# Kernel optimization log

Hardware: AMD Instinct MI355X
Metric: run time of the kernel (lower is better)

The kernel has to match this reference:

```python
import jax, jax.numpy as jnp
import numpy as np

BETA = 0.999      # EMA momentum from __init__ default
MIN_PTS = 256     # per-class minimum point count from forward()
EPS = 1e-12       # torch F.normalize eps


def _l2norm(v):
    n = jnp.sqrt(jnp.sum(v * v, axis=1, keepdims=True))
    return v / jnp.maximum(n, EPS)


def setup_inputs() -> dict:
    key = jax.random.key(0)
    ks = jax.random.split(key, 14)
    B, N, CIN = 4, 40000, 4
    ENC_H, ENC_D, PROJ_H, PRIOR_D, NC = 256, 512, 256, 128, 13
    s = 0.02
    pos = jax.random.normal(ks[0], (B, N, 3), jnp.float32)
    x = jax.random.normal(ks[1], (B, CIN, N), jnp.float32)
    y = jax.random.randint(ks[2], (B, N), 0, NC)
    # pointwise encoder stand-in (real encoder is an opaque external PointNeXt)
    W_enc1 = jax.random.normal(ks[3], (CIN + 3, ENC_H), jnp.float32) * s
    b_enc1 = jnp.zeros((ENC_H,), jnp.float32)
    W_enc2 = jax.random.normal(ks[4], (ENC_H, ENC_D), jnp.float32) * s
    b_enc2 = jnp.zeros((ENC_D,), jnp.float32)
    # projection head: Linear(512->256) ReLU Linear(256->128) ReLU
    W1 = jax.random.normal(ks[5], (ENC_D, PROJ_H), jnp.float32) * s
    b1 = jnp.zeros((PROJ_H,), jnp.float32)
    W2 = jax.random.normal(ks[6], (PROJ_H, PRIOR_D), jnp.float32) * s
    b2 = jnp.zeros((PRIOR_D,), jnp.float32)
    prior_ema = _l2norm(jax.random.uniform(ks[7], (NC, PRIOR_D), jnp.float32))
    return {"pos": pos, "x": x, "y": y,
            "W_enc1": W_enc1, "b_enc1": b_enc1, "W_enc2": W_enc2, "b_enc2": b_enc2,
            "W1": W1, "b1": b1, "W2": W2, "b2": b2, "prior_ema": prior_ema}


def reference(pos, x, y, W_enc1, b_enc1, W_enc2, b_enc2, W1, b1, W2, b2, prior_ema):
    NC = prior_ema.shape[0]
    p0 = pos.reshape(-1, pos.shape[-1])                       # [P, 3]
    f0 = jnp.transpose(x, (0, 2, 1)).reshape(-1, x.shape[1])  # [P, C]
    labels = y.reshape(-1)                                    # [P]
    # per-class counts and the >=256 validity gate (replaces the Python class loop)
    counts = jax.ops.segment_sum(jnp.ones(labels.shape, jnp.float32), labels, num_segments=NC)
    valid = counts >= MIN_PTS                                 # [NC]
    # encoder stand-in: pointwise MLP on (features, coords)
    h = jax.nn.relu(jnp.concatenate([f0, p0], axis=1) @ W_enc1 + b_enc1)
    enc = jax.nn.relu(h @ W_enc2 + b_enc2)                    # [P, 512]
    # projection head + L2 normalize
    g = jax.nn.relu(enc @ W1 + b1)
    feat = jax.nn.relu(g @ W2 + b2)                           # [P, 128]
    feat = _l2norm(feat)
    # current_prior: features + float label column (-1 marks dropped classes)
    lbl_eff = jnp.where(valid[labels], labels, -1)
    current_prior = jnp.concatenate([feat, lbl_eff[:, None].astype(feat.dtype)], axis=1)
    # _ema: detached per-class segment mean, keep old prior for empty/invalid classes
    fsg = jax.lax.stop_gradient(feat)
    sums = jax.ops.segment_sum(fsg, labels, num_segments=NC)  # [NC, 128]
    means = sums / jnp.maximum(counts, 1.0)[:, None]
    cur = jnp.where(valid[:, None], means, prior_ema)
    new_prior = _l2norm(BETA * prior_ema + (1.0 - BETA) * cur)
    return current_prior, new_prior
```

## Files before the change

### kernel.cpp

```cpp
#include <hip/hip_runtime.h>
#include <hip/hip_bf16.h>

#define P_TOTAL 160000
#define NPB     40000
#define NCLS    13
#define TP      64
#define NBLK    (P_TOTAL / TP)

typedef __attribute__((ext_vector_type(8))) short bf16x8;
typedef __attribute__((ext_vector_type(4))) float f32x4;

__device__ __forceinline__ ushort f2bf(float f) {
  union { float f; unsigned u; } v; v.f = f;
  return (ushort)((v.u + 0x8000) >> 16);
}

__device__ __forceinline__ void transpose_tile(const float* __restrict__ src,
                                               ushort* __restrict__ dst,
                                               int K, int N, int tile, ushort (*t)[33]) {
  int ntx = N >> 5;
  int n0 = (tile % ntx) << 5, k0 = (tile / ntx) << 5;
  int c = threadIdx.x & 31, r = threadIdx.x >> 5;
  #pragma unroll
  for (int rr = 0; rr < 32; rr += 8)
    t[r + rr][c] = f2bf(src[(k0 + r + rr) * N + n0 + c]);
  __syncthreads();
  #pragma unroll
  for (int rr = 0; rr < 32; rr += 8)
    dst[(n0 + r + rr) * K + k0 + c] = t[c][r + rr];
}

__global__ void prep_all_kernel(const float* __restrict__ We1, const float* __restrict__ We2,
                                const float* __restrict__ W1,  const float* __restrict__ W2,
                                const int* __restrict__ y,
                                ushort* __restrict__ WT1, ushort* __restrict__ WT2,
                                ushort* __restrict__ WT3, ushort* __restrict__ WT4,
                                int* __restrict__ counts) {
  __shared__ ushort t[32][33];
  __shared__ int h[NCLS];
  int b = blockIdx.x, tid = threadIdx.x;
  if (b < 128)       transpose_tile(We2, WT2, 256, 512, b, t);
  else if (b < 256)  transpose_tile(W1,  WT3, 512, 256, b - 128, t);
  else if (b < 288)  transpose_tile(W2,  WT4, 256, 128, b - 256, t);
  else if (b == 288) {
    for (int i = tid; i < 8192; i += 256) {
      int n = i >> 5, k = i & 31;
      WT1[i] = (k < 7) ? f2bf(We1[k * 256 + n]) : (ushort)0;
    }
  } else {
    if (tid < NCLS) h[tid] = 0;
    __syncthreads();
    for (int i = (b - 289) * 256 + tid; i < P_TOTAL; i += 127 * 256)
      atomicAdd(&h[y[i]], 1);
    __syncthreads();
    if (tid < NCLS) atomicAdd(&counts[tid], h[tid]);
  }
}

__global__ __launch_bounds__(512, 4) void main_kernel(
    const float* __restrict__ pos, const float* __restrict__ x, const int* __restrict__ y,
    const float* __restrict__ be1, const float* __restrict__ be2,
    const float* __restrict__ b1,  const float* __restrict__ b2,
    const ushort* __restrict__ WT1, const ushort* __restrict__ WT2,
    const ushort* __restrict__ WT3, const ushort* __restrict__ WT4,
    const int* __restrict__ counts, float* __restrict__ gsums, int* __restrict__ done,
    const float* __restrict__ prior, float* __restrict__ out) {
  __shared__ ushort actbuf[TP * 264];
  __shared__ ushort chunk2[2][TP * 136];
  __shared__ float  part[8 * TP];
  __shared__ float  inv_norm[TP];
  __shared__ float  lbl_eff[TP];
  __shared__ int    lbl[TP];
  __shared__ float  invn[NCLS];
  __shared__ int    is_last;

  const int tid  = threadIdx.x;
  const int wave = tid >> 6, lane = tid & 63;
  const int quad = lane >> 4, mrow = lane & 15;
  const long p0 = (long)blockIdx.x * TP;
  const int bb = (int)(p0 / NPB);
  const int n0 = (int)(p0 % NPB);
  const f32x4 zero = {0.f, 0.f, 0.f, 0.f};

  for (int i = tid; i < TP * 40; i += 512) {
    int r = i / 40, k = i - r * 40;
    float v = 0.f;
    if (k < 4)      v = x[(bb * 4 + k) * NPB + n0 + r];
    else if (k < 7) v = pos[(p0 + r) * 3 + (k - 4)];
    chunk2[0][r * 40 + k] = f2bf(v);
  }
  if (tid < TP) lbl[tid] = y[p0 + tid];
  __syncthreads();

  {
    f32x4 acc1[4][2];
    #pragma unroll
    for (int mt = 0; mt < 4; mt++) { acc1[mt][0] = zero; acc1[mt][1] = zero; }
    const int kl = quad << 3;
    bf16x8 af[4], bw[2];
    #pragma unroll
    for (int mt = 0; mt < 4; mt++)
      af[mt] = *(const bf16x8*)(&chunk2[0][0] + (mt * 16 + mrow) * 40 + kl);
    #pragma unroll
    for (int nt = 0; nt < 2; nt++)
      bw[nt] = *(const bf16x8*)(WT1 + (wave * 32 + nt * 16 + mrow) * 32 + kl);
    #pragma unroll
    for (int nt = 0; nt < 2; nt++)
      #pragma unroll
      for (int mt = 0; mt < 4; mt++)
        acc1[mt][nt] = __builtin_amdgcn_mfma_f32_16x16x32_bf16(af[mt], bw[nt], acc1[mt][nt], 0, 0, 0);
    #pragma unroll
    for (int nt = 0; nt < 2; nt++) {
      int n = wave * 32 + nt * 16 + mrow;
      float bv = be1[n];
      #pragma unroll
      for (int mt = 0; mt < 4; mt++)
        #pragma unroll
        for (int r = 0; r < 4; r++)
          actbuf[(mt * 16 + quad * 4 + r) * 264 + n] = f2bf(fmaxf(acc1[mt][nt][r] + bv, 0.f));
    }
  }
  __syncthreads();

  f32x4 acc3[4][2];
  #pragma unroll
  for (int mt = 0; mt < 4; mt++) { acc3[mt][0] = zero; acc3[mt][1] = zero; }

  for (int c = 0; c < 4; c++) {
    ushort* cb = &chunk2[c & 1][0];
    f32x4 acc2[4];
    #pragma unroll
    for (int mt = 0; mt < 4; mt++) acc2[mt] = zero;
    #pragma unroll
    for (int ks = 0; ks < 8; ks++) {
      const int kl = ks * 32 + (quad << 3);
      bf16x8 af[4];
      #pragma unroll
      for (int mt = 0; mt < 4; mt++)
        af[mt] = *(const bf16x8*)(actbuf + (mt * 16 + mrow) * 264 + kl);
      bf16x8 bw = *(const bf16x8*)(WT2 + (long)(c * 128 + wave * 16 + mrow) * 256 + kl);
      #pragma unroll
      for (int mt = 0; mt < 4; mt++)
        acc2[mt] = __builtin_amdgcn_mfma_f32_16x16x32_bf16(af[mt], bw, acc2[mt], 0, 0, 0);
    }
    {
      int lc = wave * 16 + mrow;
      float bv = be2[c * 128 + lc];
      #pragma unroll
      for (int mt = 0; mt < 4; mt++)
        #pragma unroll
        for (int r = 0; r < 4; r++)
          cb[(mt * 16 + quad * 4 + r) * 136 + lc] = f2bf(fmaxf(acc2[mt][r] + bv, 0.f));
    }
    __syncthreads();
    #pragma unroll
    for (int ks = 0; ks < 4; ks++) {
      const int kl = ks * 32 + (quad << 3);
      bf16x8 af[4], bw[2];
      #pragma unroll
      for (int mt = 0; mt < 4; mt++)
        af[mt] = *(const bf16x8*)(cb + (mt * 16 + mrow) * 136 + kl);
      #pragma unroll
      for (int nt = 0; nt < 2; nt++)
        bw[nt] = *(const bf16x8*)(WT3 + (long)(wave * 32 + nt * 16 + mrow) * 512 + c * 128 + kl);
      #pragma unroll
      for (int nt = 0; nt < 2; nt++)
        #pragma unroll
        for (int mt = 0; mt < 4; mt++)
          acc3[mt][nt] = __builtin_amdgcn_mfma_f32_16x16x32_bf16(af[mt], bw[nt], acc3[mt][nt], 0, 0, 0);
    }
  }

  #pragma unroll
  for (int nt = 0; nt < 2; nt++) {
    int n = wave * 32 + nt * 16 + mrow;
    float bv = b1[n];
    #pragma unroll
    for (int mt = 0; mt < 4; mt++)
      #pragma unroll
      for (int r = 0; r < 4; r++)
        actbuf[(mt * 16 + quad * 4 + r) * 264 + n] = f2bf(fmaxf(acc3[mt][nt][r] + bv, 0.f));
  }
  __syncthreads();

  f32x4 acc4[4];
  #pragma unroll
  for (int mt = 0; mt < 4; mt++) acc4[mt] = zero;
  #pragma unroll
  for (int ks = 0; ks < 8; ks++) {
    const int kl = ks * 32 + (quad << 3);
    bf16x8 af[4];
    #pragma unroll
    for (int mt = 0; mt < 4; mt++)
      af[mt] = *(const bf16x8*)(actbuf + (mt * 16 + mrow) * 264 + kl);
    bf16x8 bw = *(const bf16x8*)(WT4 + (long)(wave * 16 + mrow) * 256 + kl);
    #pragma unroll
    for (int mt = 0; mt < 4; mt++)
      acc4[mt] = __builtin_amdgcn_mfma_f32_16x16x32_bf16(af[mt], bw, acc4[mt], 0, 0, 0);
  }
  const int col = wave * 16 + mrow;
  float val[4][4];
  {
    float bv = b2[col];
    #pragma unroll
    for (int mt = 0; mt < 4; mt++)
      #pragma unroll
      for (int r = 0; r < 4; r++)
        val[mt][r] = fmaxf(acc4[mt][r] + bv, 0.f);
  }

  #pragma unroll
  for (int mt = 0; mt < 4; mt++)
    #pragma unroll
    for (int r = 0; r < 4; r++) {
      float s = val[mt][r] * val[mt][r];
      s += __shfl_xor(s, 1);  s += __shfl_xor(s, 2);
      s += __shfl_xor(s, 4);  s += __shfl_xor(s, 8);
      if (mrow == 0) part[wave * TP + mt * 16 + quad * 4 + r] = s;
    }
  __syncthreads();
  if (tid < TP) {
    float ss = 0.f;
    #pragma unroll
    for (int w = 0; w < 8; w++) ss += part[w * TP + tid];
    inv_norm[tid] = 1.f / fmaxf(sqrtf(ss), 1e-12f);
    int l = lbl[tid];
    lbl_eff[tid] = (counts[l] >= 256) ? (float)l : -1.f;
  }
  __syncthreads();

  float a[NCLS];
  #pragma unroll
  for (int cc = 0; cc < NCLS; cc++) a[cc] = 0.f;
  #pragma unroll
  for (int mt = 0; mt < 4; mt++)
    #pragma unroll
    for (int r = 0; r < 4; r++) {
      int R = mt * 16 + quad * 4 + r;
      float vn = val[mt][r] * inv_norm[R];
      out[(p0 + R) * 129 + col] = vn;
      int cls = lbl[R];
      #pragma unroll
      for (int cc = 0; cc < NCLS; cc++) a[cc] += (cls == cc) ? vn : 0.f;
    }
  if (tid < TP) out[(p0 + tid) * 129 + 128] = lbl_eff[tid];
  #pragma unroll
  for (int cc = 0; cc < NCLS; cc++) {
    a[cc] += __shfl_xor(a[cc], 16);
    a[cc] += __shfl_xor(a[cc], 32);
  }
  if (quad == 0)
    #pragma unroll
    for (int cc = 0; cc < NCLS; cc++) atomicAdd(&gsums[cc * 128 + col], a[cc]);

  __syncthreads();
  if (tid == 0) {
    int old = atomicAdd(done, 1);
    is_last = (old == NBLK - 1);
  }
  __syncthreads();
  if (!is_last) return;

  float* vbuf = (float*)actbuf;
  for (int i = tid; i < NCLS * 128; i += 512) {
    float g = atomicAdd(&gsums[i], 0.f);
    int cls = i >> 7;
    int cnt = counts[cls];
    float mean = g / fmaxf((float)cnt, 1.f);
    float pr = prior[i];
    float cur = (cnt >= 256) ? mean : pr;
    vbuf[i] = 0.999f * pr + 0.001f * cur;
  }
  __syncthreads();
  if (tid < NCLS) {
    float s = 0.f;
    for (int c = 0; c < 128; c++) { float t = vbuf[tid * 128 + c]; s += t * t; }
    invn[tid] = 1.f / fmaxf(sqrtf(s), 1e-12f);
  }
  __syncthreads();
  for (int i = tid; i < NCLS * 128; i += 512)
    out[(long)P_TOTAL * 129 + i] = vbuf[i] * invn[i >> 7];
}

extern "C" void kernel_launch(void* const* d_in, const int* in_sizes, int n_in,
                              void* d_out, int out_size, void* d_ws, size_t ws_size,
                              hipStream_t stream) {
  const float* pos   = (const float*)d_in[0];
  const float* x     = (const float*)d_in[1];
  const int*   y     = (const int*)  d_in[2];
  const float* We1   = (const float*)d_in[3];
  const float* be1   = (const float*)d_in[4];
  const float* We2   = (const float*)d_in[5];
  const float* be2   = (const float*)d_in[6];
  const float* W1    = (const float*)d_in[7];
  const float* b1    = (const float*)d_in[8];
  const float* W2    = (const float*)d_in[9];
  const float* b2    = (const float*)d_in[10];
  const float* prior = (const float*)d_in[11];
  float* out = (float*)d_out;

  char* ws = (char*)d_ws;
  int*    counts = (int*)   (ws + 0);
  float*  gsums  = (float*) (ws + 256);
  int*    done   = (int*)   (ws + 7168);
  ushort* WT1    = (ushort*)(ws + 8192);
  ushort* WT2    = (ushort*)(ws + 24576);
  ushort* WT3    = (ushort*)(ws + 286720);
  ushort* WT4    = (ushort*)(ws + 548864);

  hipMemsetAsync(ws, 0, 8192, stream);
  prep_all_kernel<<<416, 256, 0, stream>>>(We1, We2, W1, W2, y, WT1, WT2, WT3, WT4, counts);
  main_kernel    <<<NBLK, 512, 0, stream>>>(pos, x, y, be1, be2, b1, b2,
                                            WT1, WT2, WT3, WT4, counts, gsums, done, prior, out);
}
```

Baseline: 347.1 us.

## Switch middle GEMMs to 32x32x16 MFMA with wider chunks and LDS class sums

The encoder-layer-2 and projection-layer-1 GEMMs now use 32x32x16 bf16 MFMA instead of 16x16x32 and work in two 256-wide chunks rather than four 128-wide ones. Each weight fragment feeds two MFMAs, and a single full-width LDS buffer replaces the double-buffered chunk buffers, at the cost of an extra barrier between chunks. The per-class segment sums no longer use per-thread 13-register accumulators with shuffles. Instead they go through LDS atomics into a block-local table, which is flushed to global with sparse atomics. This aims to cut register pressure and global atomic traffic, but risks LDS atomic contention.

Measured after the change: 410.8 us. +18.3%, slower.

```diff
diff --git a/kernel.cpp b/kernel.cpp
--- a/kernel.cpp
+++ b/kernel.cpp
@@ -7,8 +7,9 @@
 #define TP      64
 #define NBLK    (P_TOTAL / TP)
 
-typedef __attribute__((ext_vector_type(8))) short bf16x8;
-typedef __attribute__((ext_vector_type(4))) float f32x4;
+typedef __attribute__((ext_vector_type(8)))  short bf16x8;
+typedef __attribute__((ext_vector_type(4)))  float f32x4;
+typedef __attribute__((ext_vector_type(16))) float f32x16;
 
 __device__ __forceinline__ ushort f2bf(float f) {
   union { float f; unsigned u; } v; v.f = f;
@@ -66,7 +67,7 @@
     const int* __restrict__ counts, float* __restrict__ gsums, int* __restrict__ done,
     const float* __restrict__ prior, float* __restrict__ out) {
   __shared__ ushort actbuf[TP * 264];
-  __shared__ ushort chunk2[2][TP * 136];
+  __shared__ ushort chunkbuf[TP * 264];
   __shared__ float  part[8 * TP];
   __shared__ float  inv_norm[TP];
   __shared__ float  lbl_eff[TP];
@@ -77,17 +78,18 @@
   const int tid  = threadIdx.x;
   const int wave = tid >> 6, lane = tid & 63;
   const int quad = lane >> 4, mrow = lane & 15;
+  const int half = lane >> 5, m32  = lane & 31;
   const long p0 = (long)blockIdx.x * TP;
   const int bb = (int)(p0 / NPB);
   const int n0 = (int)(p0 % NPB);
-  const f32x4 zero = {0.f, 0.f, 0.f, 0.f};
+  const f32x4 zero4 = {0.f, 0.f, 0.f, 0.f};
 
   for (int i = tid; i < TP * 40; i += 512) {
     int r = i / 40, k = i - r * 40;
     float v = 0.f;
     if (k < 4)      v = x[(bb * 4 + k) * NPB + n0 + r];
     else if (k < 7) v = pos[(p0 + r) * 3 + (k - 4)];
-    chunk2[0][r * 40 + k] = f2bf(v);
+    chunkbuf[r * 40 + k] = f2bf(v);
   }
   if (tid < TP) lbl[tid] = y[p0 + tid];
   __syncthreads();
@@ -95,12 +97,12 @@
   {
     f32x4 acc1[4][2];
     #pragma unroll
-    for (int mt = 0; mt < 4; mt++) { acc1[mt][0] = zero; acc1[mt][1] = zero; }
+    for (int mt = 0; mt < 4; mt++) { acc1[mt][0] = zero4; acc1[mt][1] = zero4; }
     const int kl = quad << 3;
     bf16x8 af[4], bw[2];
     #pragma unroll
     for (int mt = 0; mt < 4; mt++)
-      af[mt] = *(const bf16x8*)(&chunk2[0][0] + (mt * 16 + mrow) * 40 + kl);
+      af[mt] = *(const bf16x8*)(chunkbuf + (mt * 16 + mrow) * 40 + kl);
     #pragma unroll
     for (int nt = 0; nt < 2; nt++)
       bw[nt] = *(const bf16x8*)(WT1 + (wave * 32 + nt * 16 + mrow) * 32 + kl);
@@ -122,70 +124,63 @@
   }
   __syncthreads();
 
-  f32x4 acc3[4][2];
-  #pragma unroll
-  for (int mt = 0; mt < 4; mt++) { acc3[mt][0] = zero; acc3[mt][1] = zero; }
-
-  for (int c = 0; c < 4; c++) {
-    ushort* cb = &chunk2[c & 1][0];
-    f32x4 acc2[4];
-    #pragma unroll
-    for (int mt = 0; mt < 4; mt++) acc2[mt] = zero;
-    #pragma unroll
-    for (int ks = 0; ks < 8; ks++) {
-      const int kl = ks * 32 + (quad << 3);
-      bf16x8 af[4];
-      #pragma unroll
-      for (int mt = 0; mt < 4; mt++)
-        af[mt] = *(const bf16x8*)(actbuf + (mt * 16 + mrow) * 264 + kl);
-      bf16x8 bw = *(const bf16x8*)(WT2 + (long)(c * 128 + wave * 16 + mrow) * 256 + kl);
-      #pragma unroll
-      for (int mt = 0; mt < 4; mt++)
-        acc2[mt] = __builtin_amdgcn_mfma_f32_16x16x32_bf16(af[mt], bw, acc2[mt], 0, 0, 0);
-    }
+  f32x16 acc3[2];
+  #pragma unroll
+  for (int r = 0; r < 16; r++) { acc3[0][r] = 0.f; acc3[1][r] = 0.f; }
+
+  for (int c = 0; c < 2; c++) {
+    f32x16 acc2[2];
+    #pragma unroll
+    for (int r = 0; r < 16; r++) { acc2[0][r] = 0.f; acc2[1][r] = 0.f; }
+    #pragma unroll
+    for (int ks = 0; ks < 16; ks++) {
+      const int kl = ks * 16 + half * 8;
+      bf16x8 af0 = *(const bf16x8*)(actbuf + (m32)      * 264 + kl);
+      bf16x8 af1 = *(const bf16x8*)(actbuf + (32 + m32) * 264 + kl);
+      bf16x8 bw  = *(const bf16x8*)(WT2 + (long)(c * 256 + wave * 32 + m32) * 256 + kl);
+      acc2[0] = __builtin_amdgcn_mfma_f32_32x32x16_bf16(af0, bw, acc2[0], 0, 0, 0);
+      acc2[1] = __builtin_amdgcn_mfma_f32_32x32x16_bf16(af1, bw, acc2[1], 0, 0, 0);
+    }
+    if (c) __syncthreads();
     {
-      int lc = wave * 16 + mrow;
-      float bv = be2[c * 128 + lc];
-      #pragma unroll
-      for (int mt = 0; mt < 4; mt++)
+      int lc = wave * 32 + m32;
+      float bv = be2[c * 256 + lc];
+      #pragma unroll
+      for (int mt = 0; mt < 2; mt++)
         #pragma unroll
-        for (int r = 0; r < 4; r++)
-          cb[(mt * 16 + quad * 4 + r) * 136 + lc] = f2bf(fmaxf(acc2[mt][r] + bv, 0.f));
+        for (int r = 0; r < 16; r++) {
+          int row = mt * 32 + (r & 3) + 8 * (r >> 2) + 4 * half;
+          chunkbuf[row * 264 + lc] = f2bf(fmaxf(acc2[mt][r] + bv, 0.f));
+        }
     }
     __syncthreads();
     #pragma unroll
-    for (int ks = 0; ks < 4; ks++) {
-      const int kl = ks * 32 + (quad << 3);
-      bf16x8 af[4], bw[2];
-      #pragma unroll
-      for (int mt = 0; mt < 4; mt++)
-        af[mt] = *(const bf16x8*)(cb + (mt * 16 + mrow) * 136 + kl);
-      #pragma unroll
-      for (int nt = 0; nt < 2; nt++)
-        bw[nt] = *(const bf16x8*)(WT3 + (long)(wave * 32 + nt * 16 + mrow) * 512 + c * 128 + kl);
-      #pragma unroll
-      for (int nt = 0; nt < 2; nt++)
-        #pragma unroll
-        for (int mt = 0; mt < 4; mt++)
-          acc3[mt][nt] = __builtin_amdgcn_mfma_f32_16x16x32_bf16(af[mt], bw[nt], acc3[mt][nt], 0, 0, 0);
-    }
-  }
-
-  #pragma unroll
-  for (int nt = 0; nt < 2; nt++) {
-    int n = wave * 32 + nt * 16 + mrow;
+    for (int ks = 0; ks < 16; ks++) {
+      const int kl = ks * 16 + half * 8;
+      bf16x8 af0 = *(const bf16x8*)(chunkbuf + (m32)      * 264 + kl);
+      bf16x8 af1 = *(const bf16x8*)(chunkbuf + (32 + m32) * 264 + kl);
+      bf16x8 bw  = *(const bf16x8*)(WT3 + (long)(wave * 32 + m32) * 512 + c * 256 + kl);
+      acc3[0] = __builtin_amdgcn_mfma_f32_32x32x16_bf16(af0, bw, acc3[0], 0, 0, 0);
+      acc3[1] = __builtin_amdgcn_mfma_f32_32x32x16_bf16(af1, bw, acc3[1], 0, 0, 0);
+    }
+  }
+
+  {
+    int n = wave * 32 + m32;
     float bv = b1[n];
     #pragma unroll
-    for (int mt = 0; mt < 4; mt++)
-      #pragma unroll
-      for (int r = 0; r < 4; r++)
-        actbuf[(mt * 16 + quad * 4 + r) * 264 + n] = f2bf(fmaxf(acc3[mt][nt][r] + bv, 0.f));
+    for (int mt = 0; mt < 2; mt++)
+      #pragma unroll
+      for (int r = 0; r < 16; r++) {
+        int row = mt * 32 + (r & 3) + 8 * (r >> 2) + 4 * half;
+        actbuf[row * 264 + n] = f2bf(fmaxf(acc3[mt][r] + bv, 0.f));
+      }
   }
   __syncthreads();
 
   f32x4 acc4[4];
   #pragma unroll
-  for (int mt = 0; mt < 4; mt++) acc4[mt] = zero;
+  for (int mt = 0; mt < 4; mt++) acc4[mt] = zero4;
   #pragma unroll
   for (int ks = 0; ks < 8; ks++) {
     const int kl = ks * 32 + (quad << 3);
@@ -208,6 +203,9 @@
       for (int r = 0; r < 4; r++)
         val[mt][r] = fmaxf(acc4[mt][r] + bv, 0.f);
   }
+
+  float* cls_sums = (float*)chunkbuf;
+  for (int i = tid; i < NCLS * 128; i += 512) cls_sums[i] = 0.f;
 
   #pragma unroll
   for (int mt = 0; mt < 4; mt++)
@@ -229,9 +227,6 @@
   }
   __syncthreads();
 
-  float a[NCLS];
-  #pragma unroll
-  for (int cc = 0; cc < NCLS; cc++) a[cc] = 0.f;
   #pragma unroll
   for (int mt = 0; mt < 4; mt++)
     #pragma unroll
@@ -239,19 +234,14 @@
       int R = mt * 16 + quad * 4 + r;
       float vn = val[mt][r] * inv_norm[R];
       out[(p0 + R) * 129 + col] = vn;
-      int cls = lbl[R];
-      #pragma unroll
-      for (int cc = 0; cc < NCLS; cc++) a[cc] += (cls == cc) ? vn : 0.f;
+      atomicAdd(&cls_sums[lbl[R] * 128 + col], vn);
     }
   if (tid < TP) out[(p0 + tid) * 129 + 128] = lbl_eff[tid];
-  #pragma unroll
-  for (int cc = 0; cc < NCLS; cc++) {
-    a[cc] += __shfl_xor(a[cc], 16);
-    a[cc] += __shfl_xor(a[cc], 32);
-  }
-  if (quad == 0)
-    #pragma unroll
-    for (int cc = 0; cc < NCLS; cc++) atomicAdd(&gsums[cc * 128 + col], a[cc]);
+  __syncthreads();
+  for (int i = tid; i < NCLS * 128; i += 512) {
+    float s = cls_sums[i];
+    if (s != 0.f) atomicAdd(&gsums[i], s);
+  }
 
   __syncthreads();
   if (tid == 0) {
```
